# Performance work log

Measured on AMD Instinct MI355X. Metric: run time of the kernel, lower is better.

Reference implementation:

```python
import jax, jax.numpy as jnp
import numpy as np

TEMPERATURE = 1.0 / 0.07  # fixed (temperature_trainable=False)
B, D = 256, 65536


def setup_inputs() -> dict:
    key = jax.random.key(0)
    kA, kB = jax.random.split(key)
    feat_A = jax.random.normal(kA, (B, D), dtype=jnp.float32)
    feat_B = jax.random.normal(kB, (B, D), dtype=jnp.float32)
    # L2-normalize (standard for contrastive features; keeps exp(logits) finite)
    feat_A = feat_A / jnp.linalg.norm(feat_A, axis=-1, keepdims=True)
    feat_B = feat_B / jnp.linalg.norm(feat_B, axis=-1, keepdims=True)
    return {"feat_A": feat_A, "feat_B": feat_B}


def reference(feat_A, feat_B):
    # logits[i, j] = <A_i, B_j> * temperature   -- [B, B]
    logits = jnp.einsum("id,jd->ij", feat_A, feat_B) * TEMPERATURE
    pos_logits = jnp.diagonal(logits)  # [B]
    # margin=0.0, dcl=False, index=None -> neg_mask is all True, so
    # log(sum_j exp(logits)) is a full-row/col logsumexp (stable form of exp->sum->log)
    neg_A2B = jax.nn.logsumexp(logits, axis=1)  # A -> B classification
    neg_B2A = jax.nn.logsumexp(logits, axis=0)  # B -> A classification
    loss_A2B = jnp.mean(neg_A2B - pos_logits)
    loss_B2A = jnp.mean(neg_B2A - pos_logits)
    return (loss_A2B + loss_B2A) * 0.5
```

## Files before the change

kernel.cpp:

```cpp
#include <hip/hip_runtime.h>
#include <hip/hip_bf16.h>


#define D_DIM 65536
#define B_DIM 256
#define LDK 72

constexpr float TEMP = 1.0f / 0.07f;

typedef short short8 __attribute__((ext_vector_type(8)));
typedef float floatx4 __attribute__((ext_vector_type(4)));

__device__ inline unsigned short f2bf(float f) {
  unsigned u = __builtin_bit_cast(unsigned, f);
  unsigned rounding = 0x7fffu + ((u >> 16) & 1u);
  return (unsigned short)((u + rounding) >> 16);
}

__device__ inline void st_bf16x4(unsigned short* dst, float4 v) {
  uint2 u;
  u.x = (unsigned)f2bf(v.x) | ((unsigned)f2bf(v.y) << 16);
  u.y = (unsigned)f2bf(v.z) | ((unsigned)f2bf(v.w) << 16);
  *(uint2*)dst = u;
}

__global__ __launch_bounds__(256, 2) void gemm_splitk(
    const float* __restrict__ A, const float* __restrict__ Bm,
    float* __restrict__ partials, int Kc) {
  const int bid = blockIdx.x;
  const int mt = (bid & 1) * 128;
  const int nt = ((bid >> 1) & 1) * 128;
  const int chunk = bid >> 2;
  const size_t k0 = (size_t)chunk * (size_t)Kc;

  __shared__ unsigned short As[128][LDK];
  __shared__ unsigned short Bs[128][LDK];

  const int t = threadIdx.x;
  const int lane = t & 63;
  const int w = t >> 6;
  const int wm = (w & 1) * 64;
  const int wn = (w >> 1) * 64;

  const int lr = t >> 4;
  const int lc = (t & 15) * 4;

  const float* Abase = A + (size_t)(mt + lr) * D_DIM + k0 + lc;
  const float* Bbase = Bm + (size_t)(nt + lr) * D_DIM + k0 + lc;

  floatx4 acc[4][4];
#pragma unroll
  for (int mb = 0; mb < 4; ++mb)
#pragma unroll
    for (int nb = 0; nb < 4; ++nb) acc[mb][nb] = (floatx4)0.f;

  float4 ra[8], rb[8];
  const int nst = Kc >> 6;

#pragma unroll
  for (int p = 0; p < 8; ++p) {
    ra[p] = *(const float4*)(Abase + (size_t)p * 16 * D_DIM);
    rb[p] = *(const float4*)(Bbase + (size_t)p * 16 * D_DIM);
  }

  for (int s = 0; s < nst; ++s) {
#pragma unroll
    for (int p = 0; p < 8; ++p) {
      st_bf16x4(&As[lr + p * 16][lc], ra[p]);
      st_bf16x4(&Bs[lr + p * 16][lc], rb[p]);
    }
    __syncthreads();

    if (s + 1 < nst) {
      const float* Ap = Abase + (size_t)(s + 1) * 64;
      const float* Bp = Bbase + (size_t)(s + 1) * 64;
#pragma unroll
      for (int p = 0; p < 8; ++p) {
        ra[p] = *(const float4*)(Ap + (size_t)p * 16 * D_DIM);
        rb[p] = *(const float4*)(Bp + (size_t)p * 16 * D_DIM);
      }
    }

#pragma unroll
    for (int ks = 0; ks < 64; ks += 32) {
      short8 af[4], bf[4];
      const int ko = ks + (lane >> 4) * 8;
#pragma unroll
      for (int mb = 0; mb < 4; ++mb)
        af[mb] = *(const short8*)&As[wm + mb * 16 + (lane & 15)][ko];
#pragma unroll
      for (int nb = 0; nb < 4; ++nb)
        bf[nb] = *(const short8*)&Bs[wn + nb * 16 + (lane & 15)][ko];
#pragma unroll
      for (int mb = 0; mb < 4; ++mb)
#pragma unroll
        for (int nb = 0; nb < 4; ++nb)
          acc[mb][nb] = __builtin_amdgcn_mfma_f32_16x16x32_bf16(
              af[mb], bf[nb], acc[mb][nb], 0, 0, 0);
    }
    __syncthreads();
  }

  float* outp = partials + (size_t)chunk * (B_DIM * B_DIM);
#pragma unroll
  for (int mb = 0; mb < 4; ++mb) {
#pragma unroll
    for (int nb = 0; nb < 4; ++nb) {
      const int gi0 = mt + wm + mb * 16 + ((lane >> 4) * 4);
      const int gj = nt + wn + nb * 16 + (lane & 15);
#pragma unroll
      for (int r = 0; r < 4; ++r)
        outp[(size_t)(gi0 + r) * B_DIM + gj] = acc[mb][nb][r];
    }
  }
}

__global__ __launch_bounds__(256) void finalize(
    const float* __restrict__ partials, float* __restrict__ logits,
    float* __restrict__ rowout, unsigned int* __restrict__ counter,
    float* __restrict__ out, int C) {
  const int b = blockIdx.x;
  const int t = threadIdx.x;
  const int q = t >> 6;
  const int l = t & 63;

  __shared__ float sums[4][B_DIM];
  __shared__ float wsum[4];
  __shared__ float posv;
  __shared__ int lastflag;

  float4 s4 = make_float4(0.f, 0.f, 0.f, 0.f);
  const float* pb = partials + (size_t)b * B_DIM + 4 * l;
#pragma unroll 8
  for (int c = q; c < C; c += 4) {
    const float4 v = *(const float4*)(pb + (size_t)c * (B_DIM * B_DIM));
    s4.x += v.x;
    s4.y += v.y;
    s4.z += v.z;
    s4.w += v.w;
  }
  *(float4*)&sums[q][4 * l] = s4;
  __syncthreads();

  const float lg = (sums[0][t] + sums[1][t] + sums[2][t] + sums[3][t]) * TEMP;
  logits[b * B_DIM + t] = lg;
  if (t == b) posv = lg;

  float e = expf(lg);
#pragma unroll
  for (int off = 32; off > 0; off >>= 1) e += __shfl_down(e, off);
  if (l == 0) wsum[q] = e;
  __syncthreads();
  if (t == 0) {
    const float tot = wsum[0] + wsum[1] + wsum[2] + wsum[3];
    rowout[b] = logf(tot) - 2.f * posv;
    __threadfence();
    const unsigned old = atomicAdd(counter, 1u);
    lastflag = (((old + 1u) & 255u) == 0u);
    __threadfence();
  }
  __syncthreads();
  if (!lastflag) return;

  float csum = 0.f;
#pragma unroll 8
  for (int i = 0; i < B_DIM; ++i) csum += expf(logits[i * B_DIM + t]);
  float v = rowout[t] + logf(csum);
#pragma unroll
  for (int off = 32; off > 0; off >>= 1) v += __shfl_down(v, off);
  if (l == 0) wsum[q] = v;
  __syncthreads();
  if (t == 0)
    out[0] = (wsum[0] + wsum[1] + wsum[2] + wsum[3]) * (0.5f / 256.f);
}

extern "C" void kernel_launch(void* const* d_in, const int* in_sizes, int n_in,
                              void* d_out, int out_size, void* d_ws, size_t ws_size,
                              hipStream_t stream) {
  (void)in_sizes; (void)n_in; (void)out_size;
  const float* A = (const float*)d_in[0];
  const float* Bm = (const float*)d_in[1];
  float* out = (float*)d_out;

  const size_t per = (size_t)B_DIM * B_DIM * sizeof(float);
  int C = 128;
  while (C > 1 &&
         (size_t)(C + 1) * per + (B_DIM + 16) * sizeof(float) > ws_size)
    C >>= 1;
  const int Kc = D_DIM / C;

  float* logits = (float*)d_ws;
  float* partials = (float*)d_ws + (size_t)B_DIM * B_DIM;
  float* rowout = partials + (size_t)C * B_DIM * B_DIM;
  unsigned int* counter = (unsigned int*)(rowout + B_DIM);

  gemm_splitk<<<4 * C, 256, 0, stream>>>(A, Bm, partials, Kc);
  finalize<<<B_DIM, B_DIM, 0, stream>>>(partials, logits, rowout, counter, out,
                                        C);
}
```

Baseline: 180.1 us.

## Fuse split-K GEMM and finalize into one kernel using atomic grid barriers

```diff
diff --git a/kernel.cpp b/kernel.cpp
--- a/kernel.cpp
+++ b/kernel.cpp
@@ -5,6 +5,7 @@
 #define D_DIM 65536
 #define B_DIM 256
 #define LDK 72
+#define NFIN 64
 
 constexpr float TEMP = 1.0f / 0.07f;
 
@@ -24,9 +25,10 @@
   *(uint2*)dst = u;
 }
 
-__global__ __launch_bounds__(256, 2) void gemm_splitk(
+__global__ __launch_bounds__(256, 2) void mega(
     const float* __restrict__ A, const float* __restrict__ Bm,
-    float* __restrict__ partials, int Kc) {
+    float* __restrict__ partials, float* __restrict__ logits,
+    unsigned* __restrict__ ctr, float* __restrict__ out, int Kc, int C) {
   const int bid = blockIdx.x;
   const int mt = (bid & 1) * 128;
   const int nt = ((bid >> 1) & 1) * 128;
@@ -113,65 +115,81 @@
         outp[(size_t)(gi0 + r) * B_DIM + gj] = acc[mb][nb][r];
     }
   }
-}
-
-__global__ __launch_bounds__(256) void finalize(
-    const float* __restrict__ partials, float* __restrict__ logits,
-    float* __restrict__ rowout, unsigned int* __restrict__ counter,
-    float* __restrict__ out, int C) {
-  const int b = blockIdx.x;
-  const int t = threadIdx.x;
-  const int q = t >> 6;
-  const int l = t & 63;
-
-  __shared__ float sums[4][B_DIM];
-  __shared__ float wsum[4];
-  __shared__ float posv;
-  __shared__ int lastflag;
-
+
+  __syncthreads();
+  __shared__ unsigned srank;
+  if (t == 0)
+    srank = __hip_atomic_fetch_add(&ctr[0], 1u, __ATOMIC_ACQ_REL,
+                                   __HIP_MEMORY_SCOPE_AGENT);
+  __syncthreads();
+  const unsigned nblk = gridDim.x;
+  const unsigned nonfin = nblk - NFIN;
+  const unsigned rank = srank;
+  if (rank < nonfin) return;
+  const int r = (int)(rank - nonfin);
+
+  if (t == 0) {
+    while (__hip_atomic_load(&ctr[0], __ATOMIC_ACQUIRE,
+                             __HIP_MEMORY_SCOPE_AGENT) < nblk)
+      __builtin_amdgcn_s_sleep(2);
+  }
+  __syncthreads();
+
+  const int i = 4 * r + w;
+  const float* pb = partials + (size_t)i * B_DIM + 4 * lane;
   float4 s4 = make_float4(0.f, 0.f, 0.f, 0.f);
-  const float* pb = partials + (size_t)b * B_DIM + 4 * l;
 #pragma unroll 8
-  for (int c = q; c < C; c += 4) {
+  for (int c = 0; c < C; ++c) {
     const float4 v = *(const float4*)(pb + (size_t)c * (B_DIM * B_DIM));
     s4.x += v.x;
     s4.y += v.y;
     s4.z += v.z;
     s4.w += v.w;
   }
-  *(float4*)&sums[q][4 * l] = s4;
-  __syncthreads();
-
-  const float lg = (sums[0][t] + sums[1][t] + sums[2][t] + sums[3][t]) * TEMP;
-  logits[b * B_DIM + t] = lg;
-  if (t == b) posv = lg;
-
-  float e = expf(lg);
-#pragma unroll
-  for (int off = 32; off > 0; off >>= 1) e += __shfl_down(e, off);
-  if (l == 0) wsum[q] = e;
+  const float lg0 = s4.x * TEMP, lg1 = s4.y * TEMP;
+  const float lg2 = s4.z * TEMP, lg3 = s4.w * TEMP;
+  *(float4*)&logits[(size_t)i * B_DIM + 4 * lane] =
+      make_float4(lg0, lg1, lg2, lg3);
+  float e = expf(lg0) + expf(lg1) + expf(lg2) + expf(lg3);
+#pragma unroll
+  for (int off = 32; off > 0; off >>= 1) e += __shfl_xor(e, off);
+  const int pc = i & 3;
+  const float lsel = (pc == 0) ? lg0 : (pc == 1) ? lg1 : (pc == 2) ? lg2 : lg3;
+  const float pv = __shfl(lsel, i >> 2, 64);
+  __shared__ float warr[4];
+  if (lane == 0) warr[w] = logf(e) - 2.f * pv;
+
   __syncthreads();
   if (t == 0) {
-    const float tot = wsum[0] + wsum[1] + wsum[2] + wsum[3];
-    rowout[b] = logf(tot) - 2.f * posv;
-    __threadfence();
-    const unsigned old = atomicAdd(counter, 1u);
-    lastflag = (((old + 1u) & 255u) == 0u);
-    __threadfence();
-  }
-  __syncthreads();
-  if (!lastflag) return;
-
-  float csum = 0.f;
-#pragma unroll 8
-  for (int i = 0; i < B_DIM; ++i) csum += expf(logits[i * B_DIM + t]);
-  float v = rowout[t] + logf(csum);
-#pragma unroll
-  for (int off = 32; off > 0; off >>= 1) v += __shfl_down(v, off);
-  if (l == 0) wsum[q] = v;
-  __syncthreads();
-  if (t == 0)
-    out[0] = (wsum[0] + wsum[1] + wsum[2] + wsum[3]) * (0.5f / 256.f);
+    __hip_atomic_fetch_add(&ctr[1], 1u, __ATOMIC_ACQ_REL,
+                           __HIP_MEMORY_SCOPE_AGENT);
+    while (__hip_atomic_load(&ctr[1], __ATOMIC_ACQUIRE,
+                             __HIP_MEMORY_SCOPE_AGENT) < NFIN)
+      __builtin_amdgcn_s_sleep(2);
+  }
+  __syncthreads();
+
+  const int j = 4 * r + w;
+  float ce = 0.f;
+#pragma unroll
+  for (int k = 0; k < 4; ++k)
+    ce += expf(logits[(size_t)(4 * lane + k) * B_DIM + j]);
+#pragma unroll
+  for (int off = 32; off > 0; off >>= 1) ce += __shfl_xor(ce, off);
+  if (lane == 0) warr[w] += logf(ce);
+  __syncthreads();
+
+  if (t == 0) {
+    const float bs = warr[0] + warr[1] + warr[2] + warr[3];
+    atomicAdd((float*)(ctr + 3), bs);
+    const unsigned o3 = __hip_atomic_fetch_add(&ctr[2], 1u, __ATOMIC_ACQ_REL,
+                                               __HIP_MEMORY_SCOPE_AGENT);
+    if (o3 == NFIN - 1) {
+      const float tot = __hip_atomic_load((float*)(ctr + 3), __ATOMIC_ACQUIRE,
+                                          __HIP_MEMORY_SCOPE_AGENT);
+      out[0] = tot * (0.5f / 256.f);
+    }
+  }
 }
 
 extern "C" void kernel_launch(void* const* d_in, const int* in_sizes, int n_in,
@@ -184,17 +202,13 @@
 
   const size_t per = (size_t)B_DIM * B_DIM * sizeof(float);
   int C = 128;
-  while (C > 1 &&
-         (size_t)(C + 1) * per + (B_DIM + 16) * sizeof(float) > ws_size)
-    C >>= 1;
+  while (C > 1 && (size_t)(C + 1) * per + 16 > ws_size) C >>= 1;
   const int Kc = D_DIM / C;
 
   float* logits = (float*)d_ws;
   float* partials = (float*)d_ws + (size_t)B_DIM * B_DIM;
-  float* rowout = partials + (size_t)C * B_DIM * B_DIM;
-  unsigned int* counter = (unsigned int*)(rowout + B_DIM);
-
-  gemm_splitk<<<4 * C, 256, 0, stream>>>(A, Bm, partials, Kc);
-  finalize<<<B_DIM, B_DIM, 0, stream>>>(partials, logits, rowout, counter, out,
-                                        C);
-}
+  unsigned* ctr = (unsigned*)(partials + (size_t)C * B_DIM * B_DIM);
+
+  hipMemsetAsync(ctr, 0, 16, stream);
+  mega<<<4 * C, 256, 0, stream>>>(A, Bm, partials, logits, ctr, out, Kc, C);
+}
```

Result: slower. 200.8 us (+11.5%).
